# Kernel optimization log

Measured on AMD Instinct MI355X. Metric: run time of the kernel, lower is better.

## Reference

```python
import jax, jax.numpy as jnp
import numpy as np

N = 50000      # nodes
E = 800000     # edges (avg degree 16)
B = 8          # graphs in batch
H = 128        # hidden (message_passer out_channels)
FF = 64        # fourier_feat_dim -> fourier features have dim 2*FF
REPEATS = 4    # repeats_training
OUT = 4        # output_dim
IN_X = 5
IN_MASK = 3

def _fourier(x, M):
    # https://arxiv.org/pdf/2106.02795.pdf : [cos(xM), sin(xM)] / sqrt(2F)
    p = x @ M
    return jnp.concatenate([jnp.cos(p), jnp.sin(p)], axis=-1) / jnp.sqrt(2.0 * M.shape[1])

def _seg_mean(v, idx, n):
    s = jax.ops.segment_sum(v, idx, num_segments=n)
    c = jax.ops.segment_sum(jnp.ones((v.shape[0],), v.dtype), idx, num_segments=n)
    return s / jnp.maximum(c, 1.0)[:, None]

def setup_inputs() -> dict:
    key = jax.random.key(0)
    ks = jax.random.split(key, 16)
    x = jax.random.normal(ks[0], (N, IN_X), jnp.float32)
    x_mask = jax.random.bernoulli(ks[1], 0.1, (N, IN_MASK)).astype(jnp.float32)
    edge_index = jax.random.randint(ks[2], (2, E), 0, N)
    edge_attr = jax.random.normal(ks[3], (E, 3), jnp.float32)
    pos = jax.random.uniform(ks[4], (N, 2), jnp.float32)
    batch = jnp.sort(jax.random.randint(ks[5], (N,), 0, B))
    sampling_points = jax.random.uniform(ks[6], (2,), jnp.float32)
    fourier_mat = jax.random.normal(ks[7], (2, FF), jnp.float32)  # learnable, init N(0,1)
    W_enc = jax.random.normal(ks[8], (IN_X + IN_MASK, H), jnp.float32) * 0.1
    b_enc = jnp.zeros((H,), jnp.float32)
    W_msg = jax.random.normal(ks[9], (2 * H + 3, H), jnp.float32) * 0.05
    b_msg = jnp.zeros((H,), jnp.float32)
    W_upd = jax.random.normal(ks[10], (4 * H, H), jnp.float32) * 0.05
    b_upd = jnp.zeros((H,), jnp.float32)
    W_dec = jax.random.normal(ks[11], (H, OUT), jnp.float32) * 0.1
    b_dec = jnp.zeros((OUT,), jnp.float32)
    return dict(x=x, x_mask=x_mask, edge_index=edge_index, edge_attr=edge_attr,
                pos=pos, batch=batch, sampling_points=sampling_points,
                fourier_mat=fourier_mat, W_enc=W_enc, b_enc=b_enc,
                W_msg=W_msg, b_msg=b_msg, W_upd=W_upd, b_upd=b_upd,
                W_dec=W_dec, b_dec=b_dec)

def reference(x, x_mask, edge_index, edge_attr, pos, batch, sampling_points,
              fourier_mat, W_enc, b_enc, W_msg, b_msg, W_upd, b_upd, W_dec, b_dec):
    bc = x_mask[:, -1]                                   # 0/1 BC flag
    x_full = jnp.concatenate([x, x_mask], axis=1)        # x = concat([x, x_mask])
    keys_ff = _fourier(pos, fourier_mat)                 # input fourier features [N, 2F]
    h = jax.nn.relu(x_full @ W_enc + b_enc)              # encoder -> [N, H]

    # x_BC: scatter-mean over BC nodes per graph (computed once)
    bc_sum = jax.ops.segment_sum(h * bc[:, None], batch, num_segments=B)
    bc_cnt = jax.ops.segment_sum(bc, batch, num_segments=B)
    x_BC = bc_sum / jnp.maximum(bc_cnt, 1.0)[:, None]    # [B, H]

    x_graph = _seg_mean(h, batch, B)                     # global_mean_pool [B, H]
    src, dst = edge_index[0], edge_index[1]
    deg = jnp.maximum(jax.ops.segment_sum(jnp.ones((E,), h.dtype), dst, num_segments=N), 1.0)

    for _ in range(REPEATS):  # repeated message passing
        m = jax.nn.relu(jnp.concatenate([h[src], h[dst], edge_attr], axis=1) @ W_msg + b_msg)
        agg = jax.ops.segment_sum(m, dst, num_segments=N) / deg[:, None]  # scatter-mean
        upd_in = jnp.concatenate([h, agg, x_graph[batch], x_BC[batch]], axis=1)
        h = h + jax.nn.relu(upd_in @ W_upd + b_upd)
        x_graph = _seg_mean(h, batch, B)                 # re-pool each repeat

    decoded = h @ W_dec + b_dec                          # [N, OUT]

    # kernelized fourier-feature interpolation at the sampling point
    q = _fourier(sampling_points, fourier_mat)           # [2F]
    nq = q / jnp.linalg.norm(q)
    nk = keys_ff / jnp.linalg.norm(keys_ff, axis=1, keepdims=True)
    vals_sum = h.sum(axis=0)                             # [H]
    kwv = nk.T @ h                                       # [2F, H]
    ks_sum = nk.sum(axis=0)                              # [2F]
    enc = (vals_sum + nq @ kwv) / (N + nq @ ks_sum)      # [H]
    U_sampled = enc @ W_dec + b_dec                      # [OUT]
    # pack (U_sampled, decoded) into one array: row 0 = sampled point, rows 1: = nodes
    return jnp.concatenate([U_sampled[None, :], decoded], axis=0)
```

## Files before the change

### kernel.cpp

```cpp
#include <hip/hip_runtime.h>
#include <math.h>

#define Nn 50000
#define Ee 800000
#define Bb 8
#define ROUNDS 4
#define KWVB 512
#define SCB 196
#define AP 40
#define HP 132
#define KS 40
#define NBK 196
#define P1B 391
#define CHUNK 2047

typedef __attribute__((ext_vector_type(8))) short bf16x8;
typedef __attribute__((ext_vector_type(4))) float f32x4;

__device__ inline short f2bf(float f) {
  union { float f; unsigned u; } v; v.f = f;
  unsigned r = v.u + 0x7fff + ((v.u >> 16) & 1);
  return (short)(r >> 16);
}
__device__ inline float bf2f(short s) {
  union { float f; unsigned u; } v; v.u = ((unsigned)(unsigned short)s) << 16;
  return v.f;
}

__global__ __launch_bounds__(256) void encode_seg(
    const float* __restrict__ x, const float* __restrict__ xm,
    const int* __restrict__ batch, const float* __restrict__ W,
    const float* __restrict__ b, float* __restrict__ h,
    float* __restrict__ gsum, float* __restrict__ gcnt,
    float* __restrict__ bcsum, float* __restrict__ bccnt) {
  __shared__ float xs5[128 * 5];
  __shared__ float xm3[128 * 3];
  __shared__ float ls[Bb * 128];
  __shared__ float lb[Bb * 128];
  __shared__ float lc[Bb], lbc[Bb];
  const int t = threadIdx.x;
  const int nBase = blockIdx.x * 128;
  const int j = t & 127, half = t >> 7;
  const int base5 = nBase * 5, base3 = nBase * 3;
  for (int q = t; q < 640; q += 256) xs5[q] = (base5 + q < Nn * 5) ? x[base5 + q] : 0.f;
  for (int q = t; q < 384; q += 256) xm3[q] = (base3 + q < Nn * 3) ? xm[base3 + q] : 0.f;
  for (int q = t; q < Bb * 128; q += 256) { ls[q] = 0.f; lb[q] = 0.f; }
  if (t < Bb) { lc[t] = 0.f; lbc[t] = 0.f; }
  float Wcol[8];
#pragma unroll
  for (int k = 0; k < 8; k++) Wcol[k] = W[k * 128 + j];
  const float bj = b[j];
  __syncthreads();
  int curb = -1;
  float runh = 0.f, runb = 0.f, runc = 0.f, runbc = 0.f;
  for (int kk = 0; kk < 64; kk++) {
    int i = nBase + kk * 2 + half;
    if (i >= Nn) break;
    int li = i - nBase;
    float acc = bj;
#pragma unroll
    for (int k = 0; k < 5; k++) acc = fmaf(xs5[li * 5 + k], Wcol[k], acc);
#pragma unroll
    for (int k = 0; k < 3; k++) acc = fmaf(xm3[li * 3 + k], Wcol[5 + k], acc);
    float v = fmaxf(acc, 0.f);
    h[(size_t)i * 128 + j] = v;
    float bc = xm3[li * 3 + 2];
    int g = batch[i];
    if (g != curb) {
      if (curb >= 0) {
        atomicAdd(&ls[curb * 128 + j], runh);
        atomicAdd(&lb[curb * 128 + j], runb);
        if (j == 0) { atomicAdd(&lc[curb], runc); atomicAdd(&lbc[curb], runbc); }
      }
      curb = g; runh = runb = runc = runbc = 0.f;
    }
    runh += v; runb += v * bc;
    if (j == 0) { runc += 1.f; runbc += bc; }
  }
  if (curb >= 0) {
    atomicAdd(&ls[curb * 128 + j], runh);
    atomicAdd(&lb[curb * 128 + j], runb);
    if (j == 0) { atomicAdd(&lc[curb], runc); atomicAdd(&lbc[curb], runbc); }
  }
  __syncthreads();
  for (int q = t; q < Bb * 128; q += 256) {
    float a = ls[q], c = lb[q];
    if (a != 0.f) atomicAdd(&gsum[q], a);
    if (c != 0.f) atomicAdd(&bcsum[q], c);
  }
  if (t < Bb) { atomicAdd(&gcnt[t], lc[t]); atomicAdd(&bccnt[t], lbc[t]); }
}

__global__ __launch_bounds__(256) void split_w_kernel(
    const float* __restrict__ Wm, const float* __restrict__ Wu,
    short* __restrict__ Wmt_h, short* __restrict__ Wmt_l,
    short* __restrict__ Wut_h, short* __restrict__ Wut_l) {
  int idx = blockIdx.x * 256 + threadIdx.x;
  if (idx < 32768) {
    int k = idx & 127, n = (idx >> 7) & 127, y = idx >> 14;
    float w = Wm[(size_t)(y * 128 + k) * 128 + n];
    short hi = f2bf(w);
    Wmt_h[idx] = hi;
    Wmt_l[idx] = f2bf(w - bf2f(hi));
  } else if (idx < 65536) {
    int j = idx - 32768;
    int k = j & 255, n = j >> 8;
    float w = Wu[(size_t)k * 128 + n];
    short hi = f2bf(w);
    Wut_h[j] = hi;
    Wut_l[j] = f2bf(w - bf2f(hi));
  }
}

__global__ __launch_bounds__(256) void bkt_cnt(const int* __restrict__ ei,
                                               int* __restrict__ bktcnt) {
  __shared__ int hist[NBK];
  int t = threadIdx.x;
  for (int q = t; q < NBK; q += 256) hist[q] = 0;
  __syncthreads();
  int base = blockIdx.x * CHUNK;
  int end = base + CHUNK < Ee ? base + CHUNK : Ee;
  for (int e = base + t; e < end; e += 256) atomicAdd(&hist[ei[Ee + e] >> 8], 1);
  __syncthreads();
  for (int q = t; q < NBK; q += 256)
    if (hist[q]) atomicAdd(&bktcnt[q], hist[q]);
}
__global__ __launch_bounds__(256) void bkt_scan(const int* __restrict__ bktcnt,
                                                int* __restrict__ bktbase,
                                                int* __restrict__ bktcur) {
  __shared__ int s[256];
  int t = threadIdx.x;
  int v = (t < NBK) ? bktcnt[t] : 0;
  s[t] = v;
  __syncthreads();
  for (int off = 1; off < 256; off <<= 1) {
    int x = (t >= off) ? s[t - off] : 0;
    __syncthreads();
    s[t] += x;
    __syncthreads();
  }
  int ex = s[t] - v;
  if (t < NBK) { bktbase[t] = ex; bktcur[t] = ex; }
  if (t == NBK - 1) bktbase[NBK] = ex + v;
}
__global__ __launch_bounds__(256) void bkt_part(
    const int* __restrict__ ei, const float* __restrict__ ea,
    int* __restrict__ bktcur, int2* __restrict__ recA,
    unsigned char* __restrict__ dlo) {
  __shared__ int hist[NBK], lbase[NBK], lcur[NBK];
  int t = threadIdx.x;
  for (int q = t; q < NBK; q += 256) hist[q] = 0;
  __syncthreads();
  int base = blockIdx.x * CHUNK;
  int end = base + CHUNK < Ee ? base + CHUNK : Ee;
  for (int e = base + t; e < end; e += 256) atomicAdd(&hist[ei[Ee + e] >> 8], 1);
  __syncthreads();
  for (int q = t; q < NBK; q += 256) {
    int c = hist[q];
    lbase[q] = c ? atomicAdd(&bktcur[q], c) : 0;
    lcur[q] = 0;
  }
  __syncthreads();
  for (int e = base + t; e < end; e += 256) {
    int d = ei[Ee + e];
    int bk = d >> 8;
    int p = lbase[bk] + atomicAdd(&lcur[bk], 1);
    unsigned r0 = (unsigned)ei[e] |
                  ((unsigned)(unsigned short)f2bf(ea[3 * (size_t)e + 0]) << 16);
    unsigned r1 = (unsigned)(unsigned short)f2bf(ea[3 * (size_t)e + 1]) |
                  ((unsigned)(unsigned short)f2bf(ea[3 * (size_t)e + 2]) << 16);
    recA[p] = make_int2((int)r0, (int)r1);
    dlo[p] = (unsigned char)(d & 255);
  }
}
__global__ __launch_bounds__(256) void dst_cnt_bsum(
    const int* __restrict__ bktbase, const unsigned char* __restrict__ dlo,
    int* __restrict__ cnt, int* __restrict__ bsum) {
  __shared__ int hh[256];
  __shared__ int wsum[4];
  int t = threadIdx.x;
  hh[t] = 0;
  __syncthreads();
  int b = blockIdx.x;
  int lo = bktbase[b], hi = bktbase[b + 1];
  for (int i = lo + t; i < hi; i += 256) atomicAdd(&hh[dlo[i]], 1);
  __syncthreads();
  int d = b * 256 + t;
  int v = hh[t];
  if (d < Nn) cnt[d] = v;
#pragma unroll
  for (int off = 32; off > 0; off >>= 1) v += __shfl_down(v, off);
  if ((t & 63) == 0) wsum[t >> 6] = v;
  __syncthreads();
  if (t == 0) bsum[b] = wsum[0] + wsum[1] + wsum[2] + wsum[3];
}
__global__ __launch_bounds__(256) void scan_top_kernel(const int* __restrict__ bsum,
                                                       int* __restrict__ boff) {
  __shared__ int s[256];
  int t = threadIdx.x;
  int v = (t < SCB) ? bsum[t] : 0;
  s[t] = v;
  __syncthreads();
  for (int off = 1; off < 256; off <<= 1) {
    int x = (t >= off) ? s[t - off] : 0;
    __syncthreads();
    s[t] += x;
    __syncthreads();
  }
  boff[t] = s[t] - v;
}
__global__ __launch_bounds__(256) void apply_fin(
    const int* __restrict__ cnt, const int* __restrict__ boff,
    const int* __restrict__ bktbase, const int2* __restrict__ recA,
    const unsigned char* __restrict__ dlo,
    int* __restrict__ rowptr, float* __restrict__ invdeg,
    int2* __restrict__ rec) {
  __shared__ int s[256];
  __shared__ int cur[256];
  int t = threadIdx.x, b = blockIdx.x;
  int i = b * 256 + t;
  int v = (i < Nn) ? cnt[i] : 0;
  s[t] = v;
  __syncthreads();
  for (int off = 1; off < 256; off <<= 1) {
    int x = (t >= off) ? s[t - off] : 0;
    __syncthreads();
    s[t] += x;
    __syncthreads();
  }
  int ex = boff[b] + s[t] - v;
  if (i < Nn) {
    rowptr[i] = ex;
    invdeg[i] = 1.0f / fmaxf((float)v, 1.0f);
    if (i == Nn - 1) rowptr[Nn] = ex + v;
  }
  cur[t] = ex;
  __syncthreads();
  int lo = bktbase[b], hi = bktbase[b + 1];
  for (int ii = lo + t; ii < hi; ii += 256) {
    int dl = dlo[ii];
    int p = atomicAdd(&cur[dl], 1);
    rec[p] = recA[ii];
  }
}

__global__ __launch_bounds__(128) void gb_static_kernel(
    const float* __restrict__ bcsum, const float* __restrict__ bccnt,
    const float* __restrict__ Wu, const float* __restrict__ bu,
    float* __restrict__ gbst) {
  __shared__ float xb[128];
  int g = blockIdx.x, t = threadIdx.x;
  xb[t] = bcsum[g * 128 + t] / fmaxf(bccnt[g], 1.f);
  __syncthreads();
  float acc = bu[t];
#pragma unroll 4
  for (int k = 0; k < 128; k++) acc = fmaf(xb[k], Wu[(size_t)(384 + k) * 128 + t], acc);
  gbst[g * 128 + t] = acc;
}

__global__ __launch_bounds__(128) void gb_dyn_kernel(
    const float* __restrict__ gsum, const float* __restrict__ gcnt,
    const float* __restrict__ gbst, const float* __restrict__ Wu,
    float* __restrict__ gb) {
  __shared__ float xg[128];
  int g = blockIdx.x, t = threadIdx.x;
  xg[t] = gsum[g * 128 + t] / fmaxf(gcnt[g], 1.f);
  __syncthreads();
  float acc = gbst[g * 128 + t];
#pragma unroll 4
  for (int k = 0; k < 128; k++) acc = fmaf(xg[k], Wu[(size_t)(256 + k) * 128 + t], acc);
  gb[g * 128 + t] = acc;
}

__global__ __launch_bounds__(256) void proj_mfma(
    const float* __restrict__ h, const short* __restrict__ Wth,
    unsigned char* __restrict__ hs8, unsigned short* __restrict__ hdbf) {
  __shared__ short Ah_s[64 * AP];
  __shared__ short Bh_s[128 * AP];
  const int t = threadIdx.x;
  const int nBase = blockIdx.x * 64;
  const int yoff = blockIdx.y * 16384;
  const int wave = t >> 6, lane = t & 63;
  const int ml = lane & 15, quad = lane >> 4;
  const int ko = quad * 8;

  f32x4 acc[2][4];
#pragma unroll
  for (int nt = 0; nt < 2; nt++)
#pragma unroll
    for (int mt = 0; mt < 4; mt++)
#pragma unroll
      for (int q = 0; q < 4; q++) acc[nt][mt][q] = 0.f;

  const int arow = t >> 2;
  const int kq = (t & 3) * 8;
  const int brow = t >> 1;
  const int kc = (t & 1) * 16;
  const int nd0 = nBase + arow;
  const int nn = nd0 < Nn ? nd0 : Nn - 1;

  for (int c = 0; c < 4; c++) {
    const int k0 = c * 32;
    const float* p = &h[(size_t)nn * 128 + k0 + kq];
    float4 u0 = *(const float4*)(p + 0);
    float4 u1 = *(const float4*)(p + 4);
    const bf16x8 gb0 = *(const bf16x8*)&Wth[(size_t)yoff + brow * 128 + k0 + kc];
    const bf16x8 gb1 = *(const bf16x8*)&Wth[(size_t)yoff + brow * 128 + k0 + kc + 8];
    float xs[8] = {u0.x, u0.y, u0.z, u0.w, u1.x, u1.y, u1.z, u1.w};
    bf16x8 vh0;
#pragma unroll
    for (int j = 0; j < 8; j++) vh0[j] = f2bf(xs[j]);
    __syncthreads();
    *(bf16x8*)&Ah_s[arow * AP + kq] = vh0;
    *(bf16x8*)&Bh_s[brow * AP + kc] = gb0;
    *(bf16x8*)&Bh_s[brow * AP + kc + 8] = gb1;
    __syncthreads();
#pragma unroll
    for (int mt = 0; mt < 4; mt++) {
      const int ar = (mt * 16 + ml) * AP + ko;
      bf16x8 ah = *(const bf16x8*)&Ah_s[ar];
#pragma unroll
      for (int nt = 0; nt < 2; nt++) {
        const int br = (wave * 32 + nt * 16 + ml) * AP + ko;
        bf16x8 bh = *(const bf16x8*)&Bh_s[br];
        acc[nt][mt] = __builtin_amdgcn_mfma_f32_16x16x32_bf16(ah, bh, acc[nt][mt], 0, 0, 0);
      }
    }
  }
  if (blockIdx.y == 0) {
#pragma unroll
    for (int nt = 0; nt < 2; nt++) {
      const int ch = wave * 32 + nt * 16 + ml;
#pragma unroll
      for (int mt = 0; mt < 4; mt++) {
#pragma unroll
        for (int q = 0; q < 4; q++) {
          int nd = nBase + mt * 16 + quad * 4 + q;
          if (nd < Nn) {
            int pk = __builtin_amdgcn_cvt_pk_fp8_f32(acc[nt][mt][q], acc[nt][mt][q], 0, false);
            hs8[(size_t)nd * 128 + ch] = (unsigned char)(pk & 0xff);
          }
        }
      }
    }
  } else {
#pragma unroll
    for (int nt = 0; nt < 2; nt++) {
      const int ch = wave * 32 + nt * 16 + ml;
#pragma unroll
      for (int mt = 0; mt < 4; mt++) {
#pragma unroll
        for (int q = 0; q < 4; q++) {
          int nd = nBase + mt * 16 + quad * 4 + q;
          if (nd < Nn) hdbf[(size_t)nd * 128 + ch] = (unsigned short)f2bf(acc[nt][mt][q]);
        }
      }
    }
  }
}

__global__ __launch_bounds__(256) void agg_kernel(
    const unsigned char* __restrict__ hs8, const unsigned short* __restrict__ hdbf,
    unsigned short* __restrict__ aggbf, const int2* __restrict__ rec,
    const int* __restrict__ rowptr, const float* __restrict__ invdeg,
    const float* __restrict__ Wm, const float* __restrict__ bm) {
  int t = threadIdx.x;
  int hw = t >> 5, lane = t & 31;
  int v = blockIdx.x * 8 + hw;
  if (v >= Nn) return;
  int c0 = lane * 4;
  const float4 We0 = *(const float4*)&Wm[(size_t)256 * 128 + c0];
  const float4 We1 = *(const float4*)&Wm[(size_t)257 * 128 + c0];
  const float4 We2 = *(const float4*)&Wm[(size_t)258 * 128 + c0];
  const float4 b4  = *(const float4*)&bm[c0];
  const ushort4 hd4 = *(const ushort4*)&hdbf[(size_t)v * 128 + c0];
  const float bx = b4.x + bf2f((short)hd4.x), by = b4.y + bf2f((short)hd4.y),
              bz = b4.z + bf2f((short)hd4.z), bw = b4.w + bf2f((short)hd4.w);
  float ax = 0.f, ay = 0.f, az = 0.f, aw = 0.f;
  float ax2 = 0.f, ay2 = 0.f, az2 = 0.f, aw2 = 0.f;
  const int r0 = rowptr[v], r1 = rowptr[v + 1];
  int e = r0;
  for (; e + 2 <= r1; e += 2) {
    int2 q0 = rec[e], q1 = rec[e + 1];
    int s0 = q0.x & 0xffff, s1 = q1.x & 0xffff;
    unsigned hr0 = *(const unsigned*)&hs8[(size_t)s0 * 128 + c0];
    unsigned hr1 = *(const unsigned*)&hs8[(size_t)s1 * 128 + c0];
    float e00 = bf2f((short)(q0.x >> 16));
    float e01 = bf2f((short)(q0.y & 0xffff));
    float e02 = bf2f((short)(q0.y >> 16));
    float e10 = bf2f((short)(q1.x >> 16));
    float e11 = bf2f((short)(q1.y & 0xffff));
    float e12 = bf2f((short)(q1.y >> 16));
    float h0x = __builtin_amdgcn_cvt_f32_fp8(hr0, 0);
    float h0y = __builtin_amdgcn_cvt_f32_fp8(hr0, 1);
    float h0z = __builtin_amdgcn_cvt_f32_fp8(hr0, 2);
    float h0w = __builtin_amdgcn_cvt_f32_fp8(hr0, 3);
    float h1x = __builtin_amdgcn_cvt_f32_fp8(hr1, 0);
    float h1y = __builtin_amdgcn_cvt_f32_fp8(hr1, 1);
    float h1z = __builtin_amdgcn_cvt_f32_fp8(hr1, 2);
    float h1w = __builtin_amdgcn_cvt_f32_fp8(hr1, 3);
    ax += fmaxf(fmaf(e00, We0.x, fmaf(e01, We1.x, fmaf(e02, We2.x, h0x + bx))), 0.f);
    ay += fmaxf(fmaf(e00, We0.y, fmaf(e01, We1.y, fmaf(e02, We2.y, h0y + by))), 0.f);
    az += fmaxf(fmaf(e00, We0.z, fmaf(e01, We1.z, fmaf(e02, We2.z, h0z + bz))), 0.f);
    aw += fmaxf(fmaf(e00, We0.w, fmaf(e01, We1.w, fmaf(e02, We2.w, h0w + bw))), 0.f);
    ax2 += fmaxf(fmaf(e10, We0.x, fmaf(e11, We1.x, fmaf(e12, We2.x, h1x + bx))), 0.f);
    ay2 += fmaxf(fmaf(e10, We0.y, fmaf(e11, We1.y, fmaf(e12, We2.y, h1y + by))), 0.f);
    az2 += fmaxf(fmaf(e10, We0.z, fmaf(e11, We1.z, fmaf(e12, We2.z, h1z + bz))), 0.f);
    aw2 += fmaxf(fmaf(e10, We0.w, fmaf(e11, We1.w, fmaf(e12, We2.w, h1w + bw))), 0.f);
  }
  if (e < r1) {
    int2 q0 = rec[e];
    int s0 = q0.x & 0xffff;
    unsigned hr0 = *(const unsigned*)&hs8[(size_t)s0 * 128 + c0];
    float e00 = bf2f((short)(q0.x >> 16));
    float e01 = bf2f((short)(q0.y & 0xffff));
    float e02 = bf2f((short)(q0.y >> 16));
    float h0x = __builtin_amdgcn_cvt_f32_fp8(hr0, 0);
    float h0y = __builtin_amdgcn_cvt_f32_fp8(hr0, 1);
    float h0z = __builtin_amdgcn_cvt_f32_fp8(hr0, 2);
    float h0w = __builtin_amdgcn_cvt_f32_fp8(hr0, 3);
    ax += fmaxf(fmaf(e00, We0.x, fmaf(e01, We1.x, fmaf(e02, We2.x, h0x + bx))), 0.f);
    ay += fmaxf(fmaf(e00, We0.y, fmaf(e01, We1.y, fmaf(e02, We2.y, h0y + by))), 0.f);
    az += fmaxf(fmaf(e00, We0.z, fmaf(e01, We1.z, fmaf(e02, We2.z, h0z + bz))), 0.f);
    aw += fmaxf(fmaf(e00, We0.w, fmaf(e01, We1.w, fmaf(e02, We2.w, h0w + bw))), 0.f);
  }
  const float idg = invdeg[v];
  ushort4 o;
  o.x = (unsigned short)f2bf((ax + ax2) * idg);
  o.y = (unsigned short)f2bf((ay + ay2) * idg);
  o.z = (unsigned short)f2bf((az + az2) * idg);
  o.w = (unsigned short)f2bf((aw + aw2) * idg);
  *(ushort4*)&aggbf[(size_t)v * 128 + c0] = o;
}

__global__ __launch_bounds__(256) void updg_mfma(
    float* __restrict__ h, const unsigned short* __restrict__ aggbf,
    const int* __restrict__ batch,
    const short* __restrict__ Wth, const short* __restrict__ Wtl,
    const float* __restrict__ gb, float* __restrict__ gsum_out) {
  __shared__ short Ah_s[64 * AP], Al_s[64 * AP];
  __shared__ short Bh_s[128 * AP], Bl_s[128 * AP];
  __shared__ float gbs[Bb * 128];
  __shared__ float ls[Bb * 128];
  const int t = threadIdx.x;
  const int nBase = blockIdx.x * 64;
  *(float4*)&gbs[t * 4] = *(const float4*)&gb[t * 4];
#pragma unroll
  for (int q = 0; q < 4; q++) ls[t + q * 256] = 0.f;

  const int wave = t >> 6, lane = t & 63;
  const int ml = lane & 15, quad = lane >> 4;
  const int ko = quad * 8;

  f32x4 acc[2][4];
#pragma unroll
  for (int nt = 0; nt < 2; nt++)
#pragma unroll
    for (int mt = 0; mt < 4; mt++)
#pragma unroll
      for (int q = 0; q < 4; q++) acc[nt][mt][q] = 0.f;

  const int arow = t >> 2;
  const int kq = (t & 3) * 8;
  const int brow = t >> 1;
  const int kc = (t & 1) * 16;
  const int nd0 = nBase + arow;
  const int nn = nd0 < Nn ? nd0 : Nn - 1;

  for (int c = 0; c < 8; c++) {
    const int k0 = c * 32;
    bf16x8 vh0, vl0;
    if (c < 4) {
      const float* p = &h[(size_t)nn * 128 + k0 + kq];
      float4 u0 = *(const float4*)(p + 0);
      float4 u1 = *(const float4*)(p + 4);
      float xs[8] = {u0.x, u0.y, u0.z, u0.w, u1.x, u1.y, u1.z, u1.w};
#pragma unroll
      for (int j = 0; j < 8; j++) {
        short hi = f2bf(xs[j]);
        vh0[j] = hi; vl0[j] = f2bf(xs[j] - bf2f(hi));
      }
    } else {
      vh0 = *(const bf16x8*)&aggbf[(size_t)nn * 128 + (c - 4) * 32 + kq];
    }
    const bf16x8 gb0 = *(const bf16x8*)&Wth[(size_t)brow * 256 + k0 + kc];
    const bf16x8 gb1 = *(const bf16x8*)&Wth[(size_t)brow * 256 + k0 + kc + 8];
    const bf16x8 gl0 = *(const bf16x8*)&Wtl[(size_t)brow * 256 + k0 + kc];
    const bf16x8 gl1 = *(const bf16x8*)&Wtl[(size_t)brow * 256 + k0 + kc + 8];
    __syncthreads();
    *(bf16x8*)&Ah_s[arow * AP + kq] = vh0;
    if (c < 4) *(bf16x8*)&Al_s[arow * AP + kq] = vl0;
    *(bf16x8*)&Bh_s[brow * AP + kc] = gb0;
    *(bf16x8*)&Bh_s[brow * AP + kc + 8] = gb1;
    *(bf16x8*)&Bl_s[brow * AP + kc] = gl0;
    *(bf16x8*)&Bl_s[brow * AP + kc + 8] = gl1;
    __syncthreads();
    if (c < 4) {
#pragma unroll
      for (int mt = 0; mt < 4; mt++) {
        const int ar = (mt * 16 + ml) * AP + ko;
        bf16x8 ah = *(const bf16x8*)&Ah_s[ar];
        bf16x8 al = *(const bf16x8*)&Al_s[ar];
#pragma unroll
        for (int nt = 0; nt < 2; nt++) {
          const int br = (wave * 32 + nt * 16 + ml) * AP + ko;
          bf16x8 bh = *(const bf16x8*)&Bh_s[br];
          bf16x8 bl = *(const bf16x8*)&Bl_s[br];
          acc[nt][mt] = __builtin_amdgcn_mfma_f32_16x16x32_bf16(ah, bh, acc[nt][mt], 0, 0, 0);
          acc[nt][mt] = __builtin_amdgcn_mfma_f32_16x16x32_bf16(ah, bl, acc[nt][mt], 0, 0, 0);
          acc[nt][mt] = __builtin_amdgcn_mfma_f32_16x16x32_bf16(al, bh, acc[nt][mt], 0, 0, 0);
        }
      }
    } else {
#pragma unroll
      for (int mt = 0; mt < 4; mt++) {
        const int ar = (mt * 16 + ml) * AP + ko;
        bf16x8 ah = *(const bf16x8*)&Ah_s[ar];
#pragma unroll
        for (int nt = 0; nt < 2; nt++) {
          const int br = (wave * 32 + nt * 16 + ml) * AP + ko;
          bf16x8 bh = *(const bf16x8*)&Bh_s[br];
          bf16x8 bl = *(const bf16x8*)&Bl_s[br];
          acc[nt][mt] = __builtin_amdgcn_mfma_f32_16x16x32_bf16(ah, bh, acc[nt][mt], 0, 0, 0);
          acc[nt][mt] = __builtin_amdgcn_mfma_f32_16x16x32_bf16(ah, bl, acc[nt][mt], 0, 0, 0);
        }
      }
    }
  }
#pragma unroll
  for (int nt = 0; nt < 2; nt++) {
    const int ch = wave * 32 + nt * 16 + ml;
#pragma unroll
    for (int mt = 0; mt < 4; mt++) {
      int rbase = nBase + mt * 16 + quad * 4;
      float runv = 0.f;
      int curb = -1;
#pragma unroll
      for (int q = 0; q < 4; q++) {
        int nd = rbase + q;
        if (nd < Nn) {
          int bi = batch[nd];
          float u = fmaxf(acc[nt][mt][q] + gbs[bi * 128 + ch], 0.f);
          float hn = h[(size_t)nd * 128 + ch] + u;
          h[(size_t)nd * 128 + ch] = hn;
          if (bi != curb) {
            if (curb >= 0) atomicAdd(&ls[curb * 128 + ch], runv);
            curb = bi;
            runv = 0.f;
          }
          runv += hn;
        }
      }
      if (curb >= 0) atomicAdd(&ls[curb * 128 + ch], runv);
    }
  }
  __syncthreads();
#pragma unroll
  for (int q = 0; q < 4; q++) {
    int idx = t + q * 256;
    float v = ls[idx];
    if (v != 0.f) atomicAdd(&gsum_out[idx], v);
  }
}

__global__ __launch_bounds__(256) void kwv_kernel(
    const float* __restrict__ h, const float* __restrict__ pos,
    const float* __restrict__ Fm, const float* __restrict__ Wd,
    const float* __restrict__ bd, float* __restrict__ partial,
    float* __restrict__ ksum, float* __restrict__ out) {
  __shared__ float h_s[32 * HP];
  __shared__ short nkT[128 * KS];
  __shared__ short hT[128 * KS];
  __shared__ float wd[512];
  __shared__ float ksum_s[128];
  __shared__ float dsum[256];
  const int t = threadIdx.x;
  const int hr = t >> 3;
  const int hc = (t & 7) * 16;
  const int fg = (t & 7) * 8;
  const int wave = t >> 6, lane = t & 63;
  const int ml = lane & 15, quad = lane >> 4;
  const int ko = quad * 8;
  if (t < 128) { *(float4*)&wd[t * 4] = *(const float4*)&Wd[t * 4]; ksum_s[t] = 0.f; }
  const float bdv = bd[t & 3];
  const int dn = (t & 127) >> 2, dno = t & 3;
  const int dk0 = (t >> 7) * 64;
  f32x4 acc[2][8];
#pragma unroll
  for (int nt = 0; nt < 2; nt++)
#pragma unroll
    for (int mt = 0; mt < 8; mt++)
#pragma unroll
      for (int q = 0; q < 4; q++) acc[nt][mt][q] = 0.f;
  float klc[8], kls[8];
#pragma unroll
  for (int f = 0; f < 8; f++) { klc[f] = 0.f; kls[f] = 0.f; }

  int ptile = -1;
  const int nTiles = (Nn + 31) / 32;
  for (int tile = blockIdx.x; tile < nTiles; tile += gridDim.x) {
    const int gh = tile * 32 + hr;
    float4 hv0 = {0.f, 0.f, 0.f, 0.f}, hv1 = hv0, hv2 = hv0, hv3 = hv0;
    float cbuf[8], sbuf[8];
    if (gh < Nn) {
      const float* hp = &h[(size_t)gh * 128 + hc];
      hv0 = *(const float4*)(hp + 0);
      hv1 = *(const float4*)(hp + 4);
      hv2 = *(const float4*)(hp + 8);
      hv3 = *(const float4*)(hp + 12);
      const float px = pos[gh * 2 + 0], py = pos[gh * 2 + 1];
#pragma unroll
      for (int f = 0; f < 8; f++) {
        float p = px * Fm[fg + f] + py * Fm[64 + fg + f];
        cbuf[f] = cosf(p) * 0.125f;
        sbuf[f] = sinf(p) * 0.125f;
      }
    } else {
#pragma unroll
      for (int f = 0; f < 8; f++) { cbuf[f] = 0.f; sbuf[f] = 0.f; }
    }
    float xs[16] = {hv0.x,hv0.y,hv0.z,hv0.w, hv1.x,hv1.y,hv1.z,hv1.w,
                    hv2.x,hv2.y,hv2.z,hv2.w, hv3.x,hv3.y,hv3.z,hv3.w};
    __syncthreads();
    if (ptile >= 0 && t < 128) {
      int gn = ptile * 32 + dn;
      if (gn < Nn) out[4 + (size_t)gn * 4 + dno] = dsum[t] + dsum[t + 128] + bdv;
    }
    *(float4*)&h_s[hr * HP + hc + 0]  = hv0;
    *(float4*)&h_s[hr * HP + hc + 4]  = hv1;
    *(float4*)&h_s[hr * HP + hc + 8]  = hv2;
    *(float4*)&h_s[hr * HP + hc + 12] = hv3;
#pragma unroll
    for (int i = 0; i < 16; i++) hT[(hc + i) * KS + hr] = f2bf(xs[i]);
#pragma unroll
    for (int f = 0; f < 8; f++) {
      nkT[(fg + f) * KS + hr] = f2bf(cbuf[f]);
      nkT[(64 + fg + f) * KS + hr] = f2bf(sbuf[f]);
      klc[f] += cbuf[f];
      kls[f] += sbuf[f];
    }
    __syncthreads();
#pragma unroll
    for (int mt = 0; mt < 8; mt++) {
      bf16x8 ah = *(const bf16x8*)&nkT[(mt * 16 + ml) * KS + ko];
#pragma unroll
      for (int nt = 0; nt < 2; nt++) {
        bf16x8 bh = *(const bf16x8*)&hT[(wave * 32 + nt * 16 + ml) * KS + ko];
        acc[nt][mt] = __builtin_amdgcn_mfma_f32_16x16x32_bf16(ah, bh, acc[nt][mt], 0, 0, 0);
      }
    }
    {
      float s = 0.f;
#pragma unroll 4
      for (int kk = dk0; kk < dk0 + 64; kk++) {
        int k = (kk + dn) & 127;
        s = fmaf(h_s[dn * HP + k], wd[k * 4 + dno], s);
      }
      dsum[t] = s;
    }
    ptile = tile;
  }
  __syncthreads();
  if (ptile >= 0 && t < 128) {
    int gn = ptile * 32 + dn;
    if (gn < Nn) out[4 + (size_t)gn * 4 + dno] = dsum[t] + dsum[t + 128] + bdv;
  }
  float* pb = &partial[(size_t)blockIdx.x * 16384];
#pragma unroll
  for (int nt = 0; nt < 2; nt++) {
    const int col = wave * 32 + nt * 16 + ml;
#pragma unroll
    for (int mt = 0; mt < 8; mt++) {
#pragma unroll
      for (int q = 0; q < 4; q++) {
        int row = mt * 16 + quad * 4 + q;
        pb[row * 128 + col] = acc[nt][mt][q];
      }
    }
  }
#pragma unroll
  for (int f = 0; f < 8; f++) {
    atomicAdd(&ksum_s[fg + f], klc[f]);
    atomicAdd(&ksum_s[64 + fg + f], kls[f]);
  }
  __syncthreads();
  if (t < 128) atomicAdd(&ksum[t], ksum_s[t]);
}

__global__ __launch_bounds__(256) void kwv_reduce(const float* __restrict__ partial,
                                                  float* __restrict__ kwv) {
  int idx = blockIdx.x * 256 + threadIdx.x;
  float s = 0.f;
  for (int b = 0; b < KWVB; b++) s += partial[(size_t)b * 16384 + idx];
  kwv[idx] = s;
}

__global__ __launch_bounds__(128) void final_kernel(
    const float* __restrict__ sp, const float* __restrict__ Fm,
    const float* __restrict__ kwv, const float* __restrict__ vs,
    const float* __restrict__ ksum, const float* __restrict__ Wd,
    const float* __restrict__ bd, float* __restrict__ out) {
  __shared__ float nq_s[128];
  __shared__ float red[2];
  __shared__ float redU[8];
  int t = threadIdx.x;
  int jj = t & 63;
  float p = sp[0] * Fm[jj] + sp[1] * Fm[64 + jj];
  nq_s[t] = ((t < 64) ? cosf(p) : sinf(p)) * 0.125f;
  __syncthreads();
  float num = 0.f;
#pragma unroll
  for (int g = 0; g < Bb; g++) num += vs[g * 128 + t];
  for (int k = 0; k < 128; k++) num = fmaf(nq_s[k], kwv[k * 128 + t], num);
  float dp = nq_s[t] * ksum[t];
#pragma unroll
  for (int off = 32; off > 0; off >>= 1) dp += __shfl_down(dp, off);
  if ((t & 63) == 0) red[t >> 6] = dp;
  __syncthreads();
  float den = (float)Nn + red[0] + red[1];
  float e = num / den;
  float u[4];
#pragma unroll
  for (int o = 0; o < 4; o++) u[o] = e * Wd[t * 4 + o];
#pragma unroll
  for (int off = 32; off > 0; off >>= 1) {
#pragma unroll
    for (int o = 0; o < 4; o++) u[o] += __shfl_down(u[o], off);
  }
  if ((t & 63) == 0) {
#pragma unroll
    for (int o = 0; o < 4; o++) redU[(t >> 6) * 4 + o] = u[o];
  }
  __syncthreads();
  if (t < 4) out[t] = redU[t] + redU[4 + t] + bd[t];
}

extern "C" void kernel_launch(void* const* d_in, const int* in_sizes, int n_in,
                              void* d_out, int out_size, void* d_ws, size_t ws_size,
                              hipStream_t stream) {
  const float* x    = (const float*)d_in[0];
  const float* xm   = (const float*)d_in[1];
  const int*   ei   = (const int*)d_in[2];
  const float* ea   = (const float*)d_in[3];
  const float* pos  = (const float*)d_in[4];
  const int*   batch= (const int*)d_in[5];
  const float* sp   = (const float*)d_in[6];
  const float* Fm   = (const float*)d_in[7];
  const float* Wenc = (const float*)d_in[8];
  const float* benc = (const float*)d_in[9];
  const float* Wmsg = (const float*)d_in[10];
  const float* bmsg = (const float*)d_in[11];
  const float* Wupd = (const float*)d_in[12];
  const float* bupd = (const float*)d_in[13];
  const float* Wdec = (const float*)d_in[14];
  const float* bdec = (const float*)d_in[15];
  float* out = (float*)d_out;

  float* ws     = (float*)d_ws;
  float* h      = ws;
  float* agg    = h + (size_t)Nn * 128;
  float* aux    = agg + (size_t)Nn * 128;
  float* invdeg = aux + (size_t)Nn * 128;
  float* gsum   = invdeg + Nn;
  float* gcnt   = gsum + 1024;
  float* bcsum  = gcnt + 8;
  float* bccnt  = bcsum + 1024;
  float* gsumR  = bccnt + 8;
  float* vsum   = gsumR + 4096;
  float* ksum   = vsum + 128;
  float* gbst   = ksum + 128;
  float* gbuf   = gbst + 1024;
  float* kwv    = gbuf + 4096;
  int2*  rec    = (int2*)(kwv + 16384);
  int*   cnt    = (int*)(rec + Ee);
  int*   rowptr = cnt + Nn;
  int*   bsum   = rowptr + Nn + 1;
  int*   boff   = bsum + 256;
  int*   bktcnt = boff + 256;
  int*   bktbase= bktcnt + 196;
  int*   bktcur = bktbase + 197;
  short* wmt_h  = (short*)(bktcur + 196);
  short* wmt_l  = wmt_h + 32768;
  short* wut_h  = wmt_l + 32768;
  short* wut_l  = wut_h + 32768;
  int2*  recA   = (int2*)(wut_l + 32768);
  unsigned char* dlo = (unsigned char*)(recA + Ee);

  unsigned short* aggbf = (unsigned short*)agg;
  unsigned char*  hs8   = (unsigned char*)aux;
  unsigned short* hdbf  = (unsigned short*)(hs8 + (size_t)Nn * 128);

  hipMemsetAsync(gsum, 0, 6416 * sizeof(float), stream);
  hipMemsetAsync(bktcnt, 0, 196 * sizeof(int), stream);

  split_w_kernel<<<256, 256, 0, stream>>>(Wmsg, Wupd, wmt_h, wmt_l, wut_h, wut_l);

  bkt_cnt<<<P1B, 256, 0, stream>>>(ei, bktcnt);
  bkt_scan<<<1, 256, 0, stream>>>(bktcnt, bktbase, bktcur);
  bkt_part<<<P1B, 256, 0, stream>>>(ei, ea, bktcur, recA, dlo);
  dst_cnt_bsum<<<NBK, 256, 0, stream>>>(bktbase, dlo, cnt, bsum);
  scan_top_kernel<<<1, 256, 0, stream>>>(bsum, boff);
  apply_fin<<<NBK, 256, 0, stream>>>(cnt, boff, bktbase, recA, dlo,
                                     rowptr, invdeg, rec);

  const int nb128 = (Nn + 127) / 128;
  const int nb64  = (Nn + 63) / 64;
  encode_seg<<<nb128, 256, 0, stream>>>(x, xm, batch, Wenc, benc, h,
                                        gsum, gcnt, bcsum, bccnt);
  gb_static_kernel<<<Bb, 128, 0, stream>>>(bcsum, bccnt, Wupd, bupd, gbst);
  gb_dyn_kernel<<<Bb, 128, 0, stream>>>(gsum, gcnt, gbst, Wupd, gbuf);

  for (int r = 0; r < ROUNDS; r++) {
    proj_mfma<<<dim3(nb64, 2), 256, 0, stream>>>(h, wmt_h, hs8, hdbf);
    agg_kernel<<<(Nn + 7) / 8, 256, 0, stream>>>(hs8, hdbf, aggbf, rec, rowptr,
                                                 invdeg, Wmsg, bmsg);
    updg_mfma<<<nb64, 256, 0, stream>>>(h, aggbf, batch, wut_h, wut_l,
                                        gbuf + r * 1024, gsumR + r * 1024);
    if (r < ROUNDS - 1)
      gb_dyn_kernel<<<Bb, 128, 0, stream>>>(gsumR + r * 1024, gcnt, gbst, Wupd,
                                            gbuf + (r + 1) * 1024);
  }

  kwv_kernel<<<KWVB, 256, 0, stream>>>(h, pos, Fm, Wdec, bdec, agg, ksum, out);
  kwv_reduce<<<64, 256, 0, stream>>>(agg, kwv);
  final_kernel<<<1, 128, 0, stream>>>(sp, Fm, kwv, gsumR + 3 * 1024, ksum,
                                      Wdec, bdec, out);
}
```

Measured before the change: 643.0 us.

## Fuse small graph-bias and weight-split kernels into neighbouring launches; merge proj halves

Folds the weight bf16 split into the bucket-count kernel and the per-graph bias matvecs (static and dynamic) into the first 8 blocks of the projection kernel, removing several tiny launches and one memset. The projection kernel now computes both the src and dst halves in one block (256 weight rows staged in shared memory) instead of a 2-wide grid, so h is loaded once per round. The cost is more accumulator registers and shared memory per block, and extra serial work in the first 8 blocks.

```diff
diff --git a/kernel.cpp b/kernel.cpp
--- a/kernel.cpp
+++ b/kernel.cpp
@@ -91,11 +91,14 @@
   if (t < Bb) { atomicAdd(&gcnt[t], lc[t]); atomicAdd(&bccnt[t], lbc[t]); }
 }
 
-__global__ __launch_bounds__(256) void split_w_kernel(
+__global__ __launch_bounds__(256) void bkt_cnt(
+    const int* __restrict__ ei, int* __restrict__ bktcnt,
     const float* __restrict__ Wm, const float* __restrict__ Wu,
     short* __restrict__ Wmt_h, short* __restrict__ Wmt_l,
     short* __restrict__ Wut_h, short* __restrict__ Wut_l) {
-  int idx = blockIdx.x * 256 + threadIdx.x;
+  __shared__ int hist[NBK];
+  int t = threadIdx.x;
+  int idx = blockIdx.x * 256 + t;
   if (idx < 32768) {
     int k = idx & 127, n = (idx >> 7) & 127, y = idx >> 14;
     float w = Wm[(size_t)(y * 128 + k) * 128 + n];
@@ -110,12 +113,6 @@
     Wut_h[j] = hi;
     Wut_l[j] = f2bf(w - bf2f(hi));
   }
-}
-
-__global__ __launch_bounds__(256) void bkt_cnt(const int* __restrict__ ei,
-                                               int* __restrict__ bktcnt) {
-  __shared__ int hist[NBK];
-  int t = threadIdx.x;
   for (int q = t; q < NBK; q += 256) hist[q] = 0;
   __syncthreads();
   int base = blockIdx.x * CHUNK;
@@ -244,58 +241,55 @@
   }
 }
 
-__global__ __launch_bounds__(128) void gb_static_kernel(
-    const float* __restrict__ bcsum, const float* __restrict__ bccnt,
-    const float* __restrict__ Wu, const float* __restrict__ bu,
-    float* __restrict__ gbst) {
-  __shared__ float xb[128];
-  int g = blockIdx.x, t = threadIdx.x;
-  xb[t] = bcsum[g * 128 + t] / fmaxf(bccnt[g], 1.f);
-  __syncthreads();
-  float acc = bu[t];
-#pragma unroll 4
-  for (int k = 0; k < 128; k++) acc = fmaf(xb[k], Wu[(size_t)(384 + k) * 128 + t], acc);
-  gbst[g * 128 + t] = acc;
-}
-
-__global__ __launch_bounds__(128) void gb_dyn_kernel(
-    const float* __restrict__ gsum, const float* __restrict__ gcnt,
-    const float* __restrict__ gbst, const float* __restrict__ Wu,
-    float* __restrict__ gb) {
-  __shared__ float xg[128];
-  int g = blockIdx.x, t = threadIdx.x;
-  xg[t] = gsum[g * 128 + t] / fmaxf(gcnt[g], 1.f);
-  __syncthreads();
-  float acc = gbst[g * 128 + t];
-#pragma unroll 4
-  for (int k = 0; k < 128; k++) acc = fmaf(xg[k], Wu[(size_t)(256 + k) * 128 + t], acc);
-  gb[g * 128 + t] = acc;
-}
-
 __global__ __launch_bounds__(256) void proj_mfma(
     const float* __restrict__ h, const short* __restrict__ Wth,
-    unsigned char* __restrict__ hs8, unsigned short* __restrict__ hdbf) {
+    unsigned char* __restrict__ hs8, unsigned short* __restrict__ hdbf,
+    const float* __restrict__ bcsum, const float* __restrict__ bccnt,
+    const float* __restrict__ bu, const float* __restrict__ Wu,
+    float* __restrict__ gbst, const float* __restrict__ gsum_in,
+    const float* __restrict__ gcnt, float* __restrict__ gb_out, int dogbst) {
   __shared__ short Ah_s[64 * AP];
-  __shared__ short Bh_s[128 * AP];
+  __shared__ short Bh_s[256 * AP];
   const int t = threadIdx.x;
   const int nBase = blockIdx.x * 64;
-  const int yoff = blockIdx.y * 16384;
   const int wave = t >> 6, lane = t & 63;
   const int ml = lane & 15, quad = lane >> 4;
   const int ko = quad * 8;
 
-  f32x4 acc[2][4];
-#pragma unroll
-  for (int nt = 0; nt < 2; nt++)
+  if (blockIdx.x < Bb) {
+    float* xgs = (float*)Bh_s;
+    const int g = blockIdx.x;
+    if (dogbst) {
+      if (t < 128) xgs[t] = bcsum[g * 128 + t] / fmaxf(bccnt[g], 1.f);
+      __syncthreads();
+      if (t < 128) {
+        float a = bu[t];
+#pragma unroll 4
+        for (int k = 0; k < 128; k++) a = fmaf(xgs[k], Wu[(size_t)(384 + k) * 128 + t], a);
+        gbst[g * 128 + t] = a;
+      }
+      __syncthreads();
+    }
+    if (t < 128) xgs[t] = gsum_in[g * 128 + t] / fmaxf(gcnt[g], 1.f);
+    __syncthreads();
+    if (t < 128) {
+      float a = gbst[g * 128 + t];
+#pragma unroll 4
+      for (int k = 0; k < 128; k++) a = fmaf(xgs[k], Wu[(size_t)(256 + k) * 128 + t], a);
+      gb_out[g * 128 + t] = a;
+    }
+  }
+
+  f32x4 acc[4][4];
+#pragma unroll
+  for (int yn = 0; yn < 4; yn++)
 #pragma unroll
     for (int mt = 0; mt < 4; mt++)
 #pragma unroll
-      for (int q = 0; q < 4; q++) acc[nt][mt][q] = 0.f;
+      for (int q = 0; q < 4; q++) acc[yn][mt][q] = 0.f;
 
   const int arow = t >> 2;
   const int kq = (t & 3) * 8;
-  const int brow = t >> 1;
-  const int kc = (t & 1) * 16;
   const int nd0 = nBase + arow;
   const int nn = nd0 < Nn ? nd0 : Nn - 1;
 
@@ -304,55 +298,48 @@
     const float* p = &h[(size_t)nn * 128 + k0 + kq];
     float4 u0 = *(const float4*)(p + 0);
     float4 u1 = *(const float4*)(p + 4);
-    const bf16x8 gb0 = *(const bf16x8*)&Wth[(size_t)yoff + brow * 128 + k0 + kc];
-    const bf16x8 gb1 = *(const bf16x8*)&Wth[(size_t)yoff + brow * 128 + k0 + kc + 8];
+    const bf16x8 w0 = *(const bf16x8*)&Wth[(size_t)t * 128 + k0];
+    const bf16x8 w1 = *(const bf16x8*)&Wth[(size_t)t * 128 + k0 + 8];
+    const bf16x8 w2 = *(const bf16x8*)&Wth[(size_t)t * 128 + k0 + 16];
+    const bf16x8 w3 = *(const bf16x8*)&Wth[(size_t)t * 128 + k0 + 24];
     float xs[8] = {u0.x, u0.y, u0.z, u0.w, u1.x, u1.y, u1.z, u1.w};
     bf16x8 vh0;
 #pragma unroll
     for (int j = 0; j < 8; j++) vh0[j] = f2bf(xs[j]);
     __syncthreads();
     *(bf16x8*)&Ah_s[arow * AP + kq] = vh0;
-    *(bf16x8*)&Bh_s[brow * AP + kc] = gb0;
-    *(bf16x8*)&Bh_s[brow * AP + kc + 8] = gb1;
+    *(bf16x8*)&Bh_s[t * AP + 0] = w0;
+    *(bf16x8*)&Bh_s[t * AP + 8] = w1;
+    *(bf16x8*)&Bh_s[t * AP + 16] = w2;
+    *(bf16x8*)&Bh_s[t * AP + 24] = w3;
     __syncthreads();
 #pragma unroll
     for (int mt = 0; mt < 4; mt++) {
       const int ar = (mt * 16 + ml) * AP + ko;
       bf16x8 ah = *(const bf16x8*)&Ah_s[ar];
 #pragma unroll
-      for (int nt = 0; nt < 2; nt++) {
-        const int br = (wave * 32 + nt * 16 + ml) * AP + ko;
-        bf16x8 bh = *(const bf16x8*)&Bh_s[br];
-        acc[nt][mt] = __builtin_amdgcn_mfma_f32_16x16x32_bf16(ah, bh, acc[nt][mt], 0, 0, 0);
-      }
-    }
-  }
-  if (blockIdx.y == 0) {
-#pragma unroll
-    for (int nt = 0; nt < 2; nt++) {
-      const int ch = wave * 32 + nt * 16 + ml;
-#pragma unroll
-      for (int mt = 0; mt < 4; mt++) {
-#pragma unroll
-        for (int q = 0; q < 4; q++) {
-          int nd = nBase + mt * 16 + quad * 4 + q;
-          if (nd < Nn) {
-            int pk = __builtin_amdgcn_cvt_pk_fp8_f32(acc[nt][mt][q], acc[nt][mt][q], 0, false);
-            hs8[(size_t)nd * 128 + ch] = (unsigned char)(pk & 0xff);
-          }
+      for (int y = 0; y < 2; y++) {
+#pragma unroll
+        for (int nt = 0; nt < 2; nt++) {
+          const int br = (y * 128 + wave * 32 + nt * 16 + ml) * AP + ko;
+          bf16x8 bh = *(const bf16x8*)&Bh_s[br];
+          acc[y * 2 + nt][mt] = __builtin_amdgcn_mfma_f32_16x16x32_bf16(ah, bh, acc[y * 2 + nt][mt], 0, 0, 0);
         }
       }
     }
-  } else {
-#pragma unroll
-    for (int nt = 0; nt < 2; nt++) {
-      const int ch = wave * 32 + nt * 16 + ml;
-#pragma unroll
-      for (int mt = 0; mt < 4; mt++) {
-#pragma unroll
-        for (int q = 0; q < 4; q++) {
-          int nd = nBase + mt * 16 + quad * 4 + q;
-          if (nd < Nn) hdbf[(size_t)nd * 128 + ch] = (unsigned short)f2bf(acc[nt][mt][q]);
+  }
+#pragma unroll
+  for (int nt = 0; nt < 2; nt++) {
+    const int ch = wave * 32 + nt * 16 + ml;
+#pragma unroll
+    for (int mt = 0; mt < 4; mt++) {
+#pragma unroll
+      for (int q = 0; q < 4; q++) {
+        int nd = nBase + mt * 16 + quad * 4 + q;
+        if (nd < Nn) {
+          int pk = __builtin_amdgcn_cvt_pk_fp8_f32(acc[nt][mt][q], acc[nt][mt][q], 0, false);
+          hs8[(size_t)nd * 128 + ch] = (unsigned char)(pk & 0xff);
+          hdbf[(size_t)nd * 128 + ch] = (unsigned short)f2bf(acc[2 + nt][mt][q]);
         }
       }
     }
@@ -768,7 +755,8 @@
   float* gsumR  = bccnt + 8;
   float* vsum   = gsumR + 4096;
   float* ksum   = vsum + 128;
-  float* gbst   = ksum + 128;
+  int*   bktcnt = (int*)(ksum + 128);
+  float* gbst   = (float*)(bktcnt + 196);
   float* gbuf   = gbst + 1024;
   float* kwv    = gbuf + 4096;
   int2*  rec    = (int2*)(kwv + 16384);
@@ -776,8 +764,7 @@
   int*   rowptr = cnt + Nn;
   int*   bsum   = rowptr + Nn + 1;
   int*   boff   = bsum + 256;
-  int*   bktcnt = boff + 256;
-  int*   bktbase= bktcnt + 196;
+  int*   bktbase= boff + 256;
   int*   bktcur = bktbase + 197;
   short* wmt_h  = (short*)(bktcur + 196);
   short* wmt_l  = wmt_h + 32768;
@@ -790,12 +777,10 @@
   unsigned char*  hs8   = (unsigned char*)aux;
   unsigned short* hdbf  = (unsigned short*)(hs8 + (size_t)Nn * 128);
 
-  hipMemsetAsync(gsum, 0, 6416 * sizeof(float), stream);
-  hipMemsetAsync(bktcnt, 0, 196 * sizeof(int), stream);
-
-  split_w_kernel<<<256, 256, 0, stream>>>(Wmsg, Wupd, wmt_h, wmt_l, wut_h, wut_l);
-
-  bkt_cnt<<<P1B, 256, 0, stream>>>(ei, bktcnt);
+  hipMemsetAsync(gsum, 0, 6612 * 4, stream);
+
+  bkt_cnt<<<P1B, 256, 0, stream>>>(ei, bktcnt, Wmsg, Wupd,
+                                   wmt_h, wmt_l, wut_h, wut_l);
   bkt_scan<<<1, 256, 0, stream>>>(bktcnt, bktbase, bktcur);
   bkt_part<<<P1B, 256, 0, stream>>>(ei, ea, bktcur, recA, dlo);
   dst_cnt_bsum<<<NBK, 256, 0, stream>>>(bktbase, dlo, cnt, bsum);
@@ -807,18 +792,18 @@
   const int nb64  = (Nn + 63) / 64;
   encode_seg<<<nb128, 256, 0, stream>>>(x, xm, batch, Wenc, benc, h,
                                         gsum, gcnt, bcsum, bccnt);
-  gb_static_kernel<<<Bb, 128, 0, stream>>>(bcsum, bccnt, Wupd, bupd, gbst);
-  gb_dyn_kernel<<<Bb, 128, 0, stream>>>(gsum, gcnt, gbst, Wupd, gbuf);
 
   for (int r = 0; r < ROUNDS; r++) {
-    proj_mfma<<<dim3(nb64, 2), 256, 0, stream>>>(h, wmt_h, hs8, hdbf);
+    proj_mfma<<<nb64, 256, 0, stream>>>(
+        h, wmt_h, hs8, hdbf,
+        bcsum, bccnt, bupd, Wupd, gbst,
+        (r == 0) ? gsum : (gsumR + (size_t)(r - 1) * 1024), gcnt,
+        gbuf + (size_t)r * 1024, (r == 0) ? 1 : 0);
     agg_kernel<<<(Nn + 7) / 8, 256, 0, stream>>>(hs8, hdbf, aggbf, rec, rowptr,
                                                  invdeg, Wmsg, bmsg);
     updg_mfma<<<nb64, 256, 0, stream>>>(h, aggbf, batch, wut_h, wut_l,
-                                        gbuf + r * 1024, gsumR + r * 1024);
-    if (r < ROUNDS - 1)
-      gb_dyn_kernel<<<Bb, 128, 0, stream>>>(gsumR + r * 1024, gcnt, gbst, Wupd,
-                                            gbuf + (r + 1) * 1024);
+                                        gbuf + (size_t)r * 1024,
+                                        gsumR + (size_t)r * 1024);
   }
 
   kwv_kernel<<<KWVB, 256, 0, stream>>>(h, pos, Fm, Wdec, bdec, agg, ksum, out);
```

After: 623.7 us. 1.03x faster.
